# Kernel tuning notes

Measured on AMD Instinct MI355X. Metric: run time of the kernel, lower is better.

## Reference

```python
import jax, jax.numpy as jnp
import numpy as np

C, V, L, P, E, HM, H, M, B, T = 512, 32000, 2, 2, 8, 1024, 8, 256, 2, 1024
TOPK, RATIO = 2, 0.5


def setup_inputs() -> dict:
    key = jax.random.key(0)
    ks = iter(jax.random.split(key, 64))

    def nrm(shape, s=0.02):
        return (jax.random.normal(next(ks), shape) * s).astype(jnp.float32)

    return {
        "ids": jax.random.randint(next(ks), (B, T), 0, V, dtype=jnp.int32),
        "embed_w": nrm((V, C)),
        "mem": nrm((M, C)),
        "mp_w": nrm((2 * C, C)), "mp_b": jnp.zeros((C,), jnp.float32),
        "qkv_w": nrm((L, P, C, 3 * C)), "qkv_b": jnp.zeros((L, P, 3 * C), jnp.float32),
        "aw_w": nrm((L, P, C, H)), "aw_b": jnp.zeros((L, P, H), jnp.float32),
        "dscale": jnp.ones((L, P), jnp.float32),
        "mg_w": nrm((L, P * C, C)), "mg_b": jnp.zeros((L, C), jnp.float32),
        "ln_g": jnp.ones((L, C), jnp.float32), "ln_b": jnp.zeros((L, C), jnp.float32),
        "gw": nrm((L, C, E)), "gb": jnp.zeros((L, E), jnp.float32),
        "ew1": nrm((L, E, C, HM)), "eb1": jnp.zeros((L, E, HM), jnp.float32),
        "ew2": nrm((L, E, HM, C)), "eb2": jnp.zeros((L, E, C), jnp.float32),
        "q1w": nrm((L, C, 4 * C)), "q1b": jnp.zeros((L, 4 * C), jnp.float32),
        "q2w": nrm((L, 4 * C, 1)), "q2b": jnp.zeros((L, 1), jnp.float32),
        "errw": nrm((L, C, C)), "errb": jnp.zeros((L, C), jnp.float32),
        "ag1w": nrm((2 * C, 4 * C)), "ag1b": jnp.zeros((4 * C,), jnp.float32),
        "ag2w": nrm((4 * C, C)), "ag2b": jnp.zeros((C,), jnp.float32),
        "pscale": jnp.ones((C,), jnp.float32),
        "head_w": nrm((C, V)), "head_b": jnp.zeros((V,), jnp.float32),
    }


def _forward(ids, embed_w, mem, mp_w, mp_b, qkv_w, qkv_b, aw_w, aw_b, dscale,
             mg_w, mg_b, ln_g, ln_b, gw, gb, ew1, eb1, ew2, eb2,
             q1w, q1b, q2w, q2b, errw, errb, ag1w, ag1b, ag2w, ag2b,
             pscale, head_w, head_b):
    b, t = ids.shape
    hd = C // H
    x = embed_w[ids]                                        # [B,T,C] embedding gather
    # DynamicMemoryBank: attention over memory slots, concat retrieved
    en = jnp.einsum('btc,mc->btm', x, mem)
    ret = jnp.einsum('btm,mc->btc', jax.nn.softmax(en, -1), mem)
    x = jnp.concatenate([x, ret], -1) @ mp_w + mp_b         # memory_proj
    for l in range(L):
        x_in = x
        # IterativeReasoningBlock: stacked MetaCognitiveAttention phases
        h = x_in
        prior = None
        outs = []
        for p in range(P):
            qkv = (h @ qkv_w[l, p] + qkv_b[l, p]).reshape(b, t, 3, H, hd)
            q, k, v = (jnp.moveaxis(qkv[:, :, i], 1, 2) for i in range(3))  # [B,H,T,hd]
            aware = (h.mean(1) @ aw_w[l, p] + aw_b[l, p])[:, :, None, None]  # [B,H,1,1]
            attn = jax.nn.softmax(
                jnp.einsum('bhtd,bhsd->bhts', q, k) * (dscale[l, p] * aware), -1)
            if prior is not None:
                attn = attn + 0.3 * prior
            prior = jax.lax.stop_gradient(attn)
            o = jnp.einsum('bhts,bhsd->bthd', attn, v).reshape(b, t, C)
            h = jax.nn.silu(o)
            outs.append(h)
        merged = jnp.concatenate(outs, -1) @ mg_w[l] + mg_b[l]
        z = merged + x_in
        mu = z.mean(-1, keepdims=True)
        xn = (z - mu) / jnp.sqrt(z.var(-1, keepdims=True) + 1e-5) * ln_g[l] + ln_b[l]
        # MoE: softmax gate, top-k routing, combine (dense-equivalent math)
        scores = jax.nn.softmax(xn @ gw[l] + gb[l], -1)     # [B,T,E]
        vals, idx = jax.lax.top_k(scores, TOPK)
        w = jnp.sum(jax.nn.one_hot(idx, E, dtype=xn.dtype) * vals[..., None], axis=-2)
        eh = jnp.einsum('btc,ech->bteh', xn, ew1[l]) + eb1[l]
        eh = eh * jax.nn.silu(eh)                           # swiglu act: x*silu(x)
        ey = jnp.einsum('bteh,ehc->btec', eh, ew2[l]) + eb2[l]
        moe_out = jnp.einsum('btec,bte->btc', ey, w)
        reason = xn + moe_out * RATIO
        # IntrospectionLayer (quality estimator sees detached x)
        quality = jax.nn.sigmoid(
            jax.nn.silu(jax.lax.stop_gradient(x_in) @ q1w[l] + q1b[l]) @ q2w[l] + q2b[l])
        intro = x_in + 0.3 * ((x_in * (1.0 - quality)) @ errw[l] + errb[l])
        # AutonomousLearningGate
        gate = jnp.tanh(
            jax.nn.silu(jnp.concatenate([reason, intro], -1) @ ag1w + ag1b) @ ag2w + ag2b)
        x = reason + gate * pscale * intro
    return x @ head_w + head_b                              # [B,T,V]


def reference(ids, embed_w, mem, mp_w, mp_b, qkv_w, qkv_b, aw_w, aw_b, dscale,
              mg_w, mg_b, ln_g, ln_b, gw, gb, ew1, eb1, ew2, eb2,
              q1w, q1b, q2w, q2b, errw, errb, ag1w, ag1b, ag2w, ag2b,
              pscale, head_w, head_b):
    return _forward(ids, embed_w, mem, mp_w, mp_b, qkv_w, qkv_b, aw_w, aw_b, dscale,
                    mg_w, mg_b, ln_g, ln_b, gw, gb, ew1, eb1, ew2, eb2,
                    q1w, q1b, q2w, q2b, errw, errb, ag1w, ag1b, ag2w, ag2b,
                    pscale, head_w, head_b)
```

## Files before the change

### kernel.cpp

```cpp
#include <hip/hip_runtime.h>


#define NTOK 2048
#define CDIM 512
#define TLEN 1024
#define NB 2
#define NH 8
#define VDIM 32000

typedef __attribute__((ext_vector_type(4))) float f32x4;
typedef __attribute__((ext_vector_type(8))) __bf16 bf16x8;

#define AS1 __attribute__((address_space(1)))
#define AS3 __attribute__((address_space(3)))

__device__ __forceinline__ void g2lds16(const void* g, void* l) {
    __builtin_amdgcn_global_load_lds((const AS1 void*)g, (AS3 void*)l, 16, 0, 0);
}

__global__ __launch_bounds__(256) void gemm_bf16(
    const __bf16* __restrict__ A,
    const __bf16* __restrict__ B,
    float* __restrict__ C_, int ldc,
    const float* __restrict__ bias,
    const float* __restrict__ res, int ldres, float alpha,
    int K, int act)
{
    __shared__ __bf16 As[128 * 32];
    __shared__ __bf16 Bs[128 * 32];
    const int tid = threadIdx.x;
    const int w = tid >> 6, lane = tid & 63;
    const int m0 = blockIdx.y * 128, n0 = blockIdx.x * 128;
    const int wr = (w >> 1) * 64, wc = (w & 1) * 64;
    f32x4 acc[4][4] = {};
    const int mrow = lane & 15, kq = (lane >> 4) * 8;
    for (int k0 = 0; k0 < K; k0 += 32) {
#pragma unroll
        for (int i = 0; i < 2; ++i) {
            const int boff = w * 2048 + i * 1024 + lane * 16;
            const int row = boff >> 6;
            const int ke = (boff & 63) >> 1;
            g2lds16(A + (long)(m0 + row) * K + k0 + ke, (char*)As + (boff - lane * 16));
            g2lds16(B + (long)(n0 + row) * K + k0 + ke, (char*)Bs + (boff - lane * 16));
        }
        __syncthreads();
        bf16x8 af[4], bfr[4];
#pragma unroll
        for (int i = 0; i < 4; ++i)
            af[i] = *(const bf16x8*)(As + (wr + i * 16 + mrow) * 32 + kq);
#pragma unroll
        for (int j = 0; j < 4; ++j)
            bfr[j] = *(const bf16x8*)(Bs + (wc + j * 16 + mrow) * 32 + kq);
#pragma unroll
        for (int i = 0; i < 4; ++i)
#pragma unroll
            for (int j = 0; j < 4; ++j)
                acc[i][j] = __builtin_amdgcn_mfma_f32_16x16x32_bf16(af[i], bfr[j], acc[i][j], 0, 0, 0);
        __syncthreads();
    }
    const int col_l = lane & 15, row_l = (lane >> 4) * 4;
#pragma unroll
    for (int i = 0; i < 4; ++i)
#pragma unroll
        for (int j = 0; j < 4; ++j) {
            const int n = n0 + wc + j * 16 + col_l;
            const float bv = bias ? bias[n] : 0.f;
#pragma unroll
            for (int r = 0; r < 4; ++r) {
                const int m = m0 + wr + i * 16 + row_l + r;
                float v = acc[i][j][r] + bv;
                if (act == 1) v = v / (1.f + __expf(-v));
                else if (act == 2) v = tanhf(v);
                v *= alpha;
                if (res) v += res[(long)m * ldres + n];
                C_[(long)m * ldc + n] = v;
            }
        }
}

__global__ __launch_bounds__(256) void route_k(const int* __restrict__ eidx,
                                               int* __restrict__ offi,
                                               int* __restrict__ list,
                                               int* __restrict__ posmap)
{
    __shared__ int cnt[8], fill[8], seg[9];
    const int t = threadIdx.x;
    if (t < 8) cnt[t] = 0;
    __syncthreads();
    for (int i = t; i < NTOK * 2; i += 256) atomicAdd(&cnt[eidx[i]], 1);
    __syncthreads();
    if (t == 0) {
        int run = 0;
        for (int e = 0; e < 8; ++e) {
            seg[e] = run;
            run += (cnt[e] + 127) & ~127;
        }
        seg[8] = run;
    }
    __syncthreads();
    if (t < 8) fill[t] = seg[t];
    if (t < 9) offi[t] = seg[t];
    __syncthreads();
    for (int i = t; i < NTOK * 2; i += 256) {
        const int e = eidx[i];
        const int g = atomicAdd(&fill[e], 1);
        list[g] = i;
        posmap[i] = g;
    }
    __syncthreads();
#pragma unroll
    for (int e = 0; e < 8; ++e)
        for (int g = seg[e] + cnt[e] + t; g < seg[e + 1]; g += 256) list[g] = 0;
}

__global__ __launch_bounds__(256) void moe_g1_k(
    const __bf16* __restrict__ A,
    const __bf16* __restrict__ Bw,
    const float* __restrict__ eb1l,
    const int* __restrict__ offi,
    const int* __restrict__ list,
    __bf16* __restrict__ EHB)
{
    const int m0 = blockIdx.y * 128;
    if (m0 >= offi[8]) return;
    int e = 0;
    while (e < 7 && offi[e + 1] <= m0) ++e;
    const __bf16* B = Bw + (long)e * (1024 * 512);
    const float* bias = eb1l + e * 1024;
    __shared__ __bf16 As[128 * 32];
    __shared__ __bf16 Bs[128 * 32];
    __shared__ int toks[128];
    const int tid = threadIdx.x;
    if (tid < 128) toks[tid] = list[m0 + tid] >> 1;
    __syncthreads();
    const int w = tid >> 6, lane = tid & 63;
    const int n0 = blockIdx.x * 128;
    const int wr = (w >> 1) * 64, wc = (w & 1) * 64;
    f32x4 acc[4][4] = {};
    const int mrow = lane & 15, kq = (lane >> 4) * 8;
    for (int k0 = 0; k0 < 512; k0 += 32) {
#pragma unroll
        for (int i = 0; i < 2; ++i) {
            const int boff = w * 2048 + i * 1024 + lane * 16;
            const int row = boff >> 6;
            const int ke = (boff & 63) >> 1;
            g2lds16(A + (long)toks[row] * 512 + k0 + ke, (char*)As + (boff - lane * 16));
            g2lds16(B + (long)(n0 + row) * 512 + k0 + ke, (char*)Bs + (boff - lane * 16));
        }
        __syncthreads();
        bf16x8 af[4], bfr[4];
#pragma unroll
        for (int i = 0; i < 4; ++i)
            af[i] = *(const bf16x8*)(As + (wr + i * 16 + mrow) * 32 + kq);
#pragma unroll
        for (int j = 0; j < 4; ++j)
            bfr[j] = *(const bf16x8*)(Bs + (wc + j * 16 + mrow) * 32 + kq);
#pragma unroll
        for (int i = 0; i < 4; ++i)
#pragma unroll
            for (int j = 0; j < 4; ++j)
                acc[i][j] = __builtin_amdgcn_mfma_f32_16x16x32_bf16(af[i], bfr[j], acc[i][j], 0, 0, 0);
        __syncthreads();
    }
    const int col_l = lane & 15, row_l = (lane >> 4) * 4;
#pragma unroll
    for (int i = 0; i < 4; ++i)
#pragma unroll
        for (int j = 0; j < 4; ++j) {
            const int n = n0 + wc + j * 16 + col_l;
            const float bv = bias[n];
#pragma unroll
            for (int r = 0; r < 4; ++r) {
                const int g = m0 + wr + i * 16 + row_l + r;
                const float v = acc[i][j][r] + bv;
                EHB[(long)g * 1024 + n] = (__bf16)(v * v / (1.f + __expf(-v)));
            }
        }
}

__global__ __launch_bounds__(256) void moe_g2_k(
    const __bf16* __restrict__ A,
    const __bf16* __restrict__ Bw,
    const float* __restrict__ eb2l,
    const int* __restrict__ offi,
    float* __restrict__ EYS)
{
    const int m0 = blockIdx.y * 128;
    if (m0 >= offi[8]) return;
    int e = 0;
    while (e < 7 && offi[e + 1] <= m0) ++e;
    const __bf16* B = Bw + (long)e * (512 * 1024);
    const float* bias = eb2l + e * 512;
    __shared__ __bf16 As[128 * 32];
    __shared__ __bf16 Bs[128 * 32];
    const int tid = threadIdx.x;
    const int w = tid >> 6, lane = tid & 63;
    const int n0 = blockIdx.x * 128;
    const int wr = (w >> 1) * 64, wc = (w & 1) * 64;
    f32x4 acc[4][4] = {};
    const int mrow = lane & 15, kq = (lane >> 4) * 8;
    for (int k0 = 0; k0 < 1024; k0 += 32) {
#pragma unroll
        for (int i = 0; i < 2; ++i) {
            const int boff = w * 2048 + i * 1024 + lane * 16;
            const int row = boff >> 6;
            const int ke = (boff & 63) >> 1;
            g2lds16(A + (long)(m0 + row) * 1024 + k0 + ke, (char*)As + (boff - lane * 16));
            g2lds16(B + (long)(n0 + row) * 1024 + k0 + ke, (char*)Bs + (boff - lane * 16));
        }
        __syncthreads();
        bf16x8 af[4], bfr[4];
#pragma unroll
        for (int i = 0; i < 4; ++i)
            af[i] = *(const bf16x8*)(As + (wr + i * 16 + mrow) * 32 + kq);
#pragma unroll
        for (int j = 0; j < 4; ++j)
            bfr[j] = *(const bf16x8*)(Bs + (wc + j * 16 + mrow) * 32 + kq);
#pragma unroll
        for (int i = 0; i < 4; ++i)
#pragma unroll
            for (int j = 0; j < 4; ++j)
                acc[i][j] = __builtin_amdgcn_mfma_f32_16x16x32_bf16(af[i], bfr[j], acc[i][j], 0, 0, 0);
        __syncthreads();
    }
    const int col_l = lane & 15, row_l = (lane >> 4) * 4;
#pragma unroll
    for (int i = 0; i < 4; ++i)
#pragma unroll
        for (int j = 0; j < 4; ++j) {
            const int n = n0 + wc + j * 16 + col_l;
            const float bv = bias[n];
#pragma unroll
            for (int r = 0; r < 4; ++r) {
                const int g = m0 + wr + i * 16 + row_l + r;
                EYS[(long)g * 512 + n] = acc[i][j][r] + bv;
            }
        }
}

__global__ __launch_bounds__(256) void reason2_k(const float* __restrict__ xn,
                                                 const float* __restrict__ EYS,
                                                 const float* __restrict__ wv,
                                                 const int* __restrict__ posmap,
                                                 float* __restrict__ reason)
{
    const long i = (long)blockIdx.x * 256 + threadIdx.x;
    const long n = i >> 9;
    const int c = (int)(i & 511);
    const int g0 = posmap[n * 2], g1 = posmap[n * 2 + 1];
    const float v = wv[n * 2] * EYS[(long)g0 * 512 + c] + wv[n * 2 + 1] * EYS[(long)g1 * 512 + c];
    reason[i] = xn[i] + 0.5f * v;
}

__global__ __launch_bounds__(256) void wtrans_k(const float* __restrict__ W0,
                                                __bf16* __restrict__ Wt0, int K, int N,
                                                long sW, long sD)
{
    const float* W = W0 + (long)blockIdx.z * sW;
    __bf16* Wt = Wt0 + (long)blockIdx.z * sD;
    __shared__ float tile[64][65];
    const int k0 = blockIdx.y * 64, n0 = blockIdx.x * 64;
    const int t = threadIdx.x;
#pragma unroll
    for (int i = 0; i < 4; ++i) {
        const int r = (t >> 4) + i * 16;
        const int c = (t & 15) * 4;
        float4 v = *(const float4*)(W + (long)(k0 + r) * N + n0 + c);
        tile[r][c] = v.x; tile[r][c + 1] = v.y; tile[r][c + 2] = v.z; tile[r][c + 3] = v.w;
    }
    __syncthreads();
#pragma unroll
    for (int i = 0; i < 4; ++i) {
        const int rr = (t >> 4) + i * 16;
        const int cc = (t & 15) * 4;
        __bf16* o = Wt + (long)(n0 + rr) * K + k0 + cc;
        o[0] = (__bf16)tile[cc][rr];
        o[1] = (__bf16)tile[cc + 1][rr];
        o[2] = (__bf16)tile[cc + 2][rr];
        o[3] = (__bf16)tile[cc + 3][rr];
    }
}

__global__ __launch_bounds__(256) void cvta_k(const float* __restrict__ src, int lda, int K,
                                              __bf16* __restrict__ dst)
{
    const int row = blockIdx.x, t = threadIdx.x;
    const float* s = src + (long)row * lda;
    __bf16* d = dst + (long)row * K;
    for (int c = t * 4; c < K; c += 1024) {
        float4 v = *(const float4*)(s + c);
        d[c] = (__bf16)v.x; d[c + 1] = (__bf16)v.y; d[c + 2] = (__bf16)v.z; d[c + 3] = (__bf16)v.w;
    }
}

__global__ __launch_bounds__(256) void embed_k(const int* __restrict__ ids,
                                               const float* __restrict__ ew,
                                               float* __restrict__ x)
{
    const int n = blockIdx.x, t = threadIdx.x;
    const long r = (long)ids[n] * CDIM;
    x[(long)n * CDIM + t]       = ew[r + t];
    x[(long)n * CDIM + 256 + t] = ew[r + 256 + t];
}

__global__ __launch_bounds__(256) void smrows_k(float* __restrict__ a)
{
    const int n = blockIdx.x, t = threadIdx.x;
    __shared__ float rs[256];
    float v = a[(long)n * 256 + t];
    rs[t] = v; __syncthreads();
    for (int o = 128; o; o >>= 1) { if (t < o) rs[t] = fmaxf(rs[t], rs[t + o]); __syncthreads(); }
    const float m = rs[0]; __syncthreads();
    const float e = __expf(v - m);
    rs[t] = e; __syncthreads();
    for (int o = 128; o; o >>= 1) { if (t < o) rs[t] += rs[t + o]; __syncthreads(); }
    a[(long)n * 256 + t] = e / rs[0];
}

__global__ __launch_bounds__(256) void concat_k(const float* __restrict__ a,
                                                const float* __restrict__ b,
                                                float* __restrict__ o)
{
    const long i = (long)blockIdx.x * 256 + threadIdx.x;
    const long n = i >> 9;
    const int c = (int)(i & 511);
    o[n * 1024 + c]       = a[i];
    o[n * 1024 + 512 + c] = b[i];
}

__global__ __launch_bounds__(64) void meanp_k(const float* __restrict__ A, int lda,
                                              float* __restrict__ part)
{
    const int bid = blockIdx.x;
    const int ts = bid & 15;
    const int cg = (bid >> 4) & 7;
    const int b  = bid >> 7;
    const int c  = cg * 64 + threadIdx.x;
    const float* p = A + ((long)b * TLEN + ts * 64) * lda + c;
    float s = 0.f;
    for (int t = 0; t < 64; ++t) s += p[(long)t * lda];
    part[(long)ts * 1024 + b * 512 + c] = s;
}
__global__ __launch_bounds__(256) void meanr_k(const float* __restrict__ part,
                                               float* __restrict__ hm)
{
    const int i = blockIdx.x * 256 + threadIdx.x;
    float s = 0.f;
    for (int ts = 0; ts < 16; ++ts) s += part[ts * 1024 + i];
    hm[i] = s * (1.f / 1024.f);
}

__global__ __launch_bounds__(64) void aware_k(const float* __restrict__ hm,
                                              const float* __restrict__ aw_w,
                                              const float* __restrict__ aw_b,
                                              int lp, float* __restrict__ out)
{
    const int t = threadIdx.x;
    if (t < NB * NH) {
        const int b = t >> 3, hh = t & 7;
        const float* W = aw_w + (long)lp * CDIM * NH;
        const float* x = hm + b * CDIM;
        float s = aw_b[lp * NH + hh];
        for (int c = 0; c < CDIM; ++c) s += x[c] * W[c * NH + hh];
        out[t] = s;
    }
}

__global__ __launch_bounds__(256) void qkvprep_k(
    const float* __restrict__ qkv,
    const float* __restrict__ dscale, int lp,
    const float* __restrict__ aware,
    __bf16* __restrict__ QKB, __bf16* __restrict__ KB, __bf16* __restrict__ VTB)
{
    const int bh = blockIdx.x >> 4;
    const int tc = blockIdx.x & 15;
    const int b = bh >> 3, h = bh & 7;
    const int tid = threadIdx.x;
    const float sc = dscale[lp] * aware[bh];
    __shared__ float vt[64][68];
    const int row = tid >> 2, c0 = (tid & 3) * 16;
    const long rbase = ((long)(b * 1024 + tc * 64 + row)) * 1536 + h * 64 + c0;
    {
        bf16x8 qo[2], ko[2];
#pragma unroll
        for (int i = 0; i < 2; ++i)
#pragma unroll
            for (int jj = 0; jj < 2; ++jj) {
                const float4 qq = *(const float4*)(qkv + rbase + (i * 2 + jj) * 4);
                const float4 kk = *(const float4*)(qkv + rbase + 512 + (i * 2 + jj) * 4);
                qo[i][jj * 4 + 0] = (__bf16)(qq.x * sc);
                qo[i][jj * 4 + 1] = (__bf16)(qq.y * sc);
                qo[i][jj * 4 + 2] = (__bf16)(qq.z * sc);
                qo[i][jj * 4 + 3] = (__bf16)(qq.w * sc);
                ko[i][jj * 4 + 0] = (__bf16)kk.x;
                ko[i][jj * 4 + 1] = (__bf16)kk.y;
                ko[i][jj * 4 + 2] = (__bf16)kk.z;
                ko[i][jj * 4 + 3] = (__bf16)kk.w;
            }
        const long obase = (long)bh * 65536 + (long)(tc * 64 + row) * 64 + c0;
        *(bf16x8*)(QKB + obase) = qo[0];
        *(bf16x8*)(QKB + obase + 8) = qo[1];
        *(bf16x8*)(KB + obase) = ko[0];
        *(bf16x8*)(KB + obase + 8) = ko[1];
    }
    {
        const long vbase = ((long)(b * 1024 + tc * 64 + row)) * 1536 + 1024 + h * 64 + c0;
#pragma unroll
        for (int i = 0; i < 4; ++i) {
            const float4 v = *(const float4*)(qkv + vbase + i * 4);
            vt[row][c0 + i * 4 + 0] = v.x;
            vt[row][c0 + i * 4 + 1] = v.y;
            vt[row][c0 + i * 4 + 2] = v.z;
            vt[row][c0 + i * 4 + 3] = v.w;
        }
    }
    __syncthreads();
    {
        const int d = row;
        const int s0 = c0;
        bf16x8 o0, o1;
#pragma unroll
        for (int j = 0; j < 8; ++j) o0[j] = (__bf16)vt[s0 + j][d];
#pragma unroll
        for (int j = 0; j < 8; ++j) o1[j] = (__bf16)vt[s0 + 8 + j][d];
        __bf16* dst = VTB + (long)bh * 65536 + (long)d * 1024 + tc * 64 + s0;
        *(bf16x8*)dst = o0;
        *(bf16x8*)(dst + 8) = o1;
    }
}

#define RB 32
__global__ __launch_bounds__(256) void attn2_k(
    const __bf16* __restrict__ QKB,
    const __bf16* __restrict__ KB,
    const __bf16* __restrict__ VTB,
    __bf16* __restrict__ prior,
    int use_prior,
    float* __restrict__ outs, int out_off)
{
    __shared__ __align__(16) __bf16 qs[RB * 64];
    __shared__ __align__(16) __bf16 kv[2][128 * 64];
    __shared__ __align__(16) __bf16 ss[RB * 1024];
    const int tid = threadIdx.x;
    const int w = tid >> 6, lane = tid & 63;
    const int rb = blockIdx.x & 31;
    const int bh = blockIdx.x >> 5;
    const int b = bh >> 3, h = bh & 7;
    const int t0 = rb * RB;
    const long qkbase = (long)bh * 65536;
    const int mrow = lane & 15, kq = (lane >> 4) * 8;

    {
        const int row = tid >> 3, gl = tid & 7;
        const int gs = gl ^ (row & 7);
        g2lds16(QKB + qkbase + (long)(t0 + row) * 64 + gs * 8,
                (char*)qs + tid * 16 - lane * 16);
    }
    {
        for (int it = 0; it < 4; ++it) {
            const int idx = it * 256 + tid;
            const int row = idx >> 3, gl = idx & 7;
            const int gs = gl ^ (row & 7);
            g2lds16(KB + qkbase + (long)row * 64 + gs * 8,
                    (char*)kv[0] + idx * 16 - lane * 16);
        }
        __syncthreads();
        int buf = 0;
        const int ntb = w * 2;
        for (int c = 0; c < 8; ++c) {
            if (c < 7) {
                const int s0n = (c + 1) * 128;
                for (int it = 0; it < 4; ++it) {
                    const int idx = it * 256 + tid;
                    const int row = idx >> 3, gl = idx & 7;
                    const int gs = gl ^ (row & 7);
                    g2lds16(KB + qkbase + (long)(s0n + row) * 64 + gs * 8,
                            (char*)kv[buf ^ 1] + idx * 16 - lane * 16);
                }
            }
            f32x4 accs[2][2] = {};
#pragma unroll
            for (int k0 = 0; k0 < 64; k0 += 32) {
                bf16x8 aq[2], bk[2];
#pragma unroll
                for (int mt = 0; mt < 2; ++mt) {
                    const int r = mt * 16 + mrow;
                    const int col = k0 + kq;
                    aq[mt] = *(const bf16x8*)(qs + r * 64 + (((col >> 3) ^ (r & 7)) << 3));
                }
#pragma unroll
                for (int j = 0; j < 2; ++j) {
                    const int nl = (ntb + j) * 16 + mrow;
                    const int col = k0 + kq;
                    bk[j] = *(const bf16x8*)(kv[buf] + nl * 64 + (((col >> 3) ^ (nl & 7)) << 3));
                }
#pragma unroll
                for (int mt = 0; mt < 2; ++mt)
#pragma unroll
                    for (int j = 0; j < 2; ++j)
                        accs[mt][j] = __builtin_amdgcn_mfma_f32_16x16x32_bf16(aq[mt], bk[j], accs[mt][j], 0, 0, 0);
            }
            const int col_l = lane & 15, row_l = (lane >> 4) * 4;
#pragma unroll
            for (int mt = 0; mt < 2; ++mt)
#pragma unroll
                for (int j = 0; j < 2; ++j) {
                    const int ccol = c * 128 + (ntb + j) * 16 + col_l;
#pragma unroll
                    for (int r = 0; r < 4; ++r) {
                        const int rr = mt * 16 + row_l + r;
                        ss[rr * 1024 + (((ccol >> 3) ^ (rr & 7)) << 3) + (ccol & 7)] = (__bf16)accs[mt][j][r];
                    }
                }
            __syncthreads();
            buf ^= 1;
        }
    }
    for (int it = 0; it < 4; ++it) {
        const int idx = it * 256 + tid;
        const int d = idx >> 4, gl = idx & 15;
        const int gs = gl ^ (d & 7);
        g2lds16(VTB + (long)bh * 65536 + (long)d * 1024 + gs * 8,
                (char*)kv[0] + idx * 16 - lane * 16);
    }
    {
        const int r = tid >> 3;
        const int li = tid & 7;
        const int rsw = r & 7;
        float mx = -1e30f;
        for (int j = 0; j < 16; ++j) {
            const int c = j * 64 + li * 8;
            bf16x8 v = *(const bf16x8*)(ss + r * 1024 + (((c >> 3) ^ rsw) << 3));
#pragma unroll
            for (int q = 0; q < 8; ++q) mx = fmaxf(mx, (float)v[q]);
        }
        mx = fmaxf(mx, __shfl_xor(mx, 1));
        mx = fmaxf(mx, __shfl_xor(mx, 2));
        mx = fmaxf(mx, __shfl_xor(mx, 4));
        float sum = 0.f;
        for (int j = 0; j < 16; ++j) {
            const int c = j * 64 + li * 8;
            __bf16* p = ss + r * 1024 + (((c >> 3) ^ rsw) << 3);
            bf16x8 v = *(const bf16x8*)p;
            bf16x8 e;
#pragma unroll
            for (int q = 0; q < 8; ++q) {
                const float ev = __expf((float)v[q] - mx);
                sum += ev;
                e[q] = (__bf16)ev;
            }
            *(bf16x8*)p = e;
        }
        sum += __shfl_xor(sum, 1);
        sum += __shfl_xor(sum, 2);
        sum += __shfl_xor(sum, 4);
        const float rinv = 1.f / sum;
        const long pbase = ((long)bh * 1024 + t0 + r) * 1024;
        for (int j = 0; j < 16; ++j) {
            const int c = j * 64 + li * 8;
            __bf16* p = ss + r * 1024 + (((c >> 3) ^ rsw) << 3);
            bf16x8 v = *(const bf16x8*)p;
            bf16x8 o;
            if (use_prior) {
                bf16x8 pr = *(const bf16x8*)(prior + pbase + c);
#pragma unroll
                for (int q = 0; q < 8; ++q)
                    o[q] = (__bf16)((float)v[q] * rinv + 0.3f * (float)pr[q]);
            } else {
#pragma unroll
                for (int q = 0; q < 8; ++q)
                    o[q] = (__bf16)((float)v[q] * rinv);
            }
            *(bf16x8*)p = o;
            *(bf16x8*)(prior + pbase + c) = o;
        }
    }
    __syncthreads();
    {
        f32x4 po[2] = {};
        int buf = 0;
        const int mt = w >> 1;
        const int ntb2 = (w & 1) * 2;
        for (int c = 0; c < 8; ++c) {
            if (c < 7) {
                const int s0n = (c + 1) * 128;
                for (int it = 0; it < 4; ++it) {
                    const int idx = it * 256 + tid;
                    const int d = idx >> 4, gl = idx & 15;
                    const int gs = gl ^ (d & 7);
                    g2lds16(VTB + (long)bh * 65536 + (long)d * 1024 + s0n + gs * 8,
                            (char*)kv[buf ^ 1] + idx * 16 - lane * 16);
                }
            }
#pragma unroll
            for (int ks = 0; ks < 4; ++ks) {
                const int r = mt * 16 + mrow;
                const int cola = c * 128 + ks * 32 + kq;
                bf16x8 pa = *(const bf16x8*)(ss + r * 1024 + (((cola >> 3) ^ (r & 7)) << 3));
                bf16x8 vb[2];
#pragma unroll
                for (int j = 0; j < 2; ++j) {
                    const int d = (ntb2 + j) * 16 + mrow;
                    const int colv = ks * 32 + kq;
                    vb[j] = *(const bf16x8*)(kv[buf] + d * 128 + (((colv >> 3) ^ (d & 7)) << 3));
                }
                po[0] = __builtin_amdgcn_mfma_f32_16x16x32_bf16(pa, vb[0], po[0], 0, 0, 0);
                po[1] = __builtin_amdgcn_mfma_f32_16x16x32_bf16(pa, vb[1], po[1], 0, 0, 0);
            }
            __syncthreads();
            buf ^= 1;
        }
        const int col_l = lane & 15, row_l = (lane >> 4) * 4;
#pragma unroll
        for (int j = 0; j < 2; ++j) {
            const int d = out_off + h * 64 + (ntb2 + j) * 16 + col_l;
#pragma unroll
            for (int r = 0; r < 4; ++r) {
                const int trow = t0 + mt * 16 + row_l + r;
                float v = po[j][r];
                v = v / (1.f + __expf(-v));
                outs[((long)(b * 1024 + trow)) * 1024 + d] = v;
            }
        }
    }
}

__global__ __launch_bounds__(256) void ln_k(const float* __restrict__ z,
                                            const float* __restrict__ g,
                                            const float* __restrict__ bb,
                                            float* __restrict__ xn)
{
    const int n = blockIdx.x, t = threadIdx.x;
    __shared__ float rs[256], rq[256];
    const float v0 = z[(long)n * 512 + t];
    const float v1 = z[(long)n * 512 + 256 + t];
    rs[t] = v0 + v1;
    rq[t] = v0 * v0 + v1 * v1;
    __syncthreads();
    for (int o = 128; o; o >>= 1) {
        if (t < o) { rs[t] += rs[t + o]; rq[t] += rq[t + o]; }
        __syncthreads();
    }
    const float mu = rs[0] * (1.f / 512.f);
    const float var = rq[0] * (1.f / 512.f) - mu * mu;
    const float rstd = rsqrtf(var + 1e-5f);
    xn[(long)n * 512 + t]       = (v0 - mu) * rstd * g[t] + bb[t];
    xn[(long)n * 512 + 256 + t] = (v1 - mu) * rstd * g[t + 256] + bb[t + 256];
}

__global__ __launch_bounds__(64) void gate_k(const float* __restrict__ xn,
                                             const float* __restrict__ gw,
                                             const float* __restrict__ gb,
                                             int l, float* __restrict__ wv,
                                             int* __restrict__ eidx)
{
    const int n = blockIdx.x, t = threadIdx.x;
    const int e = t & 7, ch = t >> 3;
    const float* W = gw + (long)l * CDIM * 8;
    float part = 0.f;
    for (int k = ch * 64; k < ch * 64 + 64; ++k) part += xn[(long)n * CDIM + k] * W[k * 8 + e];
    part += __shfl_xor(part, 8, 64);
    part += __shfl_xor(part, 16, 64);
    part += __shfl_xor(part, 32, 64);
    __shared__ float lg[8];
    if (t < 8) lg[t] = part + gb[l * 8 + t];
    __syncthreads();
    if (t == 0) {
        float m = lg[0];
        for (int i = 1; i < 8; ++i) m = fmaxf(m, lg[i]);
        float p[8], s = 0.f;
        for (int i = 0; i < 8; ++i) { p[i] = __expf(lg[i] - m); s += p[i]; }
        const float inv = 1.f / s;
        int i0 = 0;
        for (int i = 1; i < 8; ++i) if (p[i] > p[i0]) i0 = i;
        int i1 = (i0 == 0) ? 1 : 0;
        for (int i = 0; i < 8; ++i) { if (i == i0) continue; if (p[i] > p[i1]) i1 = i; }
        eidx[n * 2] = i0; eidx[n * 2 + 1] = i1;
        wv[n * 2] = p[i0] * inv; wv[n * 2 + 1] = p[i1] * inv;
    }
}

__global__ __launch_bounds__(256) void qual_k(const float* __restrict__ t1,
                                              const float* __restrict__ q2w,
                                              const float* __restrict__ q2b,
                                              int l, float* __restrict__ qual)
{
    const int n = blockIdx.x, t = threadIdx.x;
    const float* W = q2w + (long)l * 2048;
    float s = 0.f;
    for (int k = t; k < 2048; k += 256) s += t1[(long)n * 2048 + k] * W[k];
    __shared__ float rs[256];
    rs[t] = s; __syncthreads();
    for (int o = 128; o; o >>= 1) { if (t < o) rs[t] += rs[t + o]; __syncthreads(); }
    if (t == 0) {
        const float q = rs[0] + q2b[l];
        qual[n] = 1.f / (1.f + __expf(-q));
    }
}

__global__ __launch_bounds__(256) void xq_k(const float* __restrict__ x_in,
                                            const float* __restrict__ qual,
                                            float* __restrict__ xq)
{
    const long i = (long)blockIdx.x * 256 + threadIdx.x;
    const long n = i >> 9;
    xq[i] = x_in[i] * (1.f - qual[n]);
}

__global__ __launch_bounds__(256) void final_k(const float* __restrict__ reason,
                                               const float* __restrict__ gate,
                                               const float* __restrict__ pscale,
                                               const float* __restrict__ intro,
                                               float* __restrict__ xo)
{
    const long i = (long)blockIdx.x * 256 + threadIdx.x;
    const int c = (int)(i & 511);
    xo[i] = reason[i] + gate[i] * pscale[c] * intro[i];
}

extern "C" void kernel_launch(void* const* d_in, const int* in_sizes, int n_in,
                              void* d_out, int out_size, void* d_ws, size_t ws_size,
                              hipStream_t stream)
{
    (void)in_sizes; (void)n_in; (void)out_size; (void)ws_size;
    const int*   ids     = (const int*)  d_in[0];
    const float* embed_w = (const float*)d_in[1];
    const float* mem     = (const float*)d_in[2];
    const float* mp_w    = (const float*)d_in[3];
    const float* mp_b    = (const float*)d_in[4];
    const float* qkv_w   = (const float*)d_in[5];
    const float* qkv_b   = (const float*)d_in[6];
    const float* aw_w    = (const float*)d_in[7];
    const float* aw_b    = (const float*)d_in[8];
    const float* dscale  = (const float*)d_in[9];
    const float* mg_w    = (const float*)d_in[10];
    const float* mg_b    = (const float*)d_in[11];
    const float* ln_g    = (const float*)d_in[12];
    const float* ln_b    = (const float*)d_in[13];
    const float* gw      = (const float*)d_in[14];
    const float* gb      = (const float*)d_in[15];
    const float* ew1     = (const float*)d_in[16];
    const float* eb1     = (const float*)d_in[17];
    const float* ew2     = (const float*)d_in[18];
    const float* eb2     = (const float*)d_in[19];
    const float* q1w     = (const float*)d_in[20];
    const float* q1b     = (const float*)d_in[21];
    const float* q2w     = (const float*)d_in[22];
    const float* q2b     = (const float*)d_in[23];
    const float* errw    = (const float*)d_in[24];
    const float* errb    = (const float*)d_in[25];
    const float* ag1w    = (const float*)d_in[26];
    const float* ag1b    = (const float*)d_in[27];
    const float* ag2w    = (const float*)d_in[28];
    const float* ag2b    = (const float*)d_in[29];
    const float* pscale  = (const float*)d_in[30];
    const float* head_w  = (const float*)d_in[31];
    const float* head_b  = (const float*)d_in[32];
    float* out = (float*)d_out;
    float* ws  = (float*)d_ws;

    const long NC = (long)NTOK * CDIM;
    float* X0   = ws;
    float* X1   = ws + NC;
    float* RET  = ws + 2 * NC;
    float* XCAT = ws + 3 * NC;
    float* QKV  = ws + 5 * NC;
    float* OUTS = ws + 8 * NC;
    float* EN   = ws + 10 * NC;
    float* SM   = ws + 10 * NC + NC / 2;
    float* PART = SM;
    float* HMEAN= SM + 16384;
    float* AWARE= SM + 17408;
    float* QUAL = SM + 17472;
    float* WV   = SM + 19520;
    int*   EIDX = (int*)(SM + 23616);
    int*   OFFI = (int*)(SM + 27712);
    int*   LIST = (int*)(SM + 27728);
    int*   POSMAP = (int*)(SM + 32848);
    float* R      = ws + 11 * NC;
    __bf16* PRIORB = (__bf16*)R;
    float* Z      = R;
    float* XN     = R + NC;
    float* REASON = R + 2 * NC;
    float* INTRO  = R + 3 * NC;
    float* XQ     = R + 4 * NC;
    float* GATEB  = R + 5 * NC;
    __bf16* EHB   = (__bf16*)(R + 6 * NC);
    float* EYS    = R + 9 * NC;
    float* Q1B    = R + 12 * NC;

    __bf16* bfw = (__bf16*)(ws + 27 * NC);
    __bf16* WB_mp   = bfw;
    __bf16* WB_qkv  = bfw + 524288;
    __bf16* WB_mg   = bfw + 3670016;
    __bf16* WB_q1   = bfw + 4718592;
    __bf16* WB_err  = bfw + 6815744;
    __bf16* WB_ag1  = bfw + 7340032;
    __bf16* WB_ag2  = bfw + 9437184;
    __bf16* WB_memn = bfw + 10485760;
    __bf16* WB_memt = bfw + 10616832;
    __bf16* WB_head = bfw + 10747904;
    __bf16* ABF     = bfw + 27131904;
    __bf16* WB_e1   = bfw + 31326208;
    __bf16* WB_e2   = bfw + 39714816;
    __bf16* QKB = ABF;
    __bf16* KB  = ABF + 1048576;
    __bf16* VTB = ABF + 2097152;

    auto wtransN = [&](const float* W, __bf16* Wt, int K, int N, int cnt, long sW, long sD) {
        wtrans_k<<<dim3(N / 64, K / 64, cnt), 256, 0, stream>>>(W, Wt, K, N, sW, sD);
    };
    auto gemm = [&](const float* Asrc, int lda, const __bf16* B, float* C_, int ldc,
                    const float* bias, const float* res, int ldres, float alpha,
                    int Nn, int K, int act) {
        cvta_k<<<NTOK, 256, 0, stream>>>(Asrc, lda, K, ABF);
        gemm_bf16<<<dim3(Nn / 128, NTOK / 128), 256, 0, stream>>>(
            ABF, B, C_, ldc, bias, res, ldres, alpha, K, act);
    };

    wtransN(mp_w, WB_mp, 1024, 512, 1, 0, 0);
    wtransN(qkv_w, WB_qkv, 512, 1536, 4, 512 * 1536, 1536 * 512);
    wtransN(mg_w, WB_mg, 1024, 512, 2, 1024 * 512, 512 * 1024);
    wtransN(q1w, WB_q1, 512, 2048, 2, 512 * 2048, 2048 * 512);
    wtransN(errw, WB_err, 512, 512, 2, 512 * 512, 512 * 512);
    wtransN(ew1, WB_e1, 512, 1024, 16, 524288, 524288);
    wtransN(ew2, WB_e2, 1024, 512, 16, 524288, 524288);
    wtransN(ag1w, WB_ag1, 1024, 2048, 1, 0, 0);
    wtransN(ag2w, WB_ag2, 2048, 512, 1, 0, 0);
    wtransN(head_w, WB_head, 512, VDIM, 1, 0, 0);
    wtransN(mem, WB_memt, 256, 512, 1, 0, 0);
    cvta_k<<<256, 256, 0, stream>>>(mem, 512, 512, WB_memn);

    embed_k<<<NTOK, 256, 0, stream>>>(ids, embed_w, X0);
    gemm(X0, 512, WB_memn, EN, 256, nullptr, nullptr, 0, 1.f, 256, 512, 0);
    smrows_k<<<NTOK, 256, 0, stream>>>(EN);
    gemm(EN, 256, WB_memt, RET, 512, nullptr, nullptr, 0, 1.f, 512, 256, 0);
    concat_k<<<4096, 256, 0, stream>>>(X0, RET, XCAT);
    gemm(XCAT, 1024, WB_mp, X0, 512, mp_b, nullptr, 0, 1.f, 512, 1024, 0);

    float* xcur = X0;
    float* xalt = X1;
    for (int l = 0; l < 2; ++l) {
        for (int p = 0; p < 2; ++p) {
            const int lp = l * 2 + p;
            const float* hptr = (p == 0) ? xcur : OUTS;
            const int hlda = (p == 0) ? 512 : 1024;
            gemm(hptr, hlda, WB_qkv + (long)lp * 1536 * 512, QKV, 1536,
                 qkv_b + (long)lp * 1536, nullptr, 0, 1.f, 1536, 512, 0);
            meanp_k<<<256, 64, 0, stream>>>(hptr, hlda, PART);
            meanr_k<<<4, 256, 0, stream>>>(PART, HMEAN);
            aware_k<<<1, 64, 0, stream>>>(HMEAN, aw_w, aw_b, lp, AWARE);
            qkvprep_k<<<256, 256, 0, stream>>>(QKV, dscale, lp, AWARE, QKB, KB, VTB);
            attn2_k<<<512, 256, 0, stream>>>(QKB, KB, VTB, PRIORB,
                                             (p == 1) ? 1 : 0, OUTS, p * CDIM);
        }
        gemm(OUTS, 1024, WB_mg + (long)l * 512 * 1024, Z, 512, mg_b + (long)l * 512,
             xcur, 512, 1.f, 512, 1024, 0);
        ln_k<<<NTOK, 256, 0, stream>>>(Z, ln_g + (long)l * 512, ln_b + (long)l * 512, XN);
        gate_k<<<NTOK, 64, 0, stream>>>(XN, gw, gb, l, WV, EIDX);
        route_k<<<1, 256, 0, stream>>>(EIDX, OFFI, LIST, POSMAP);
        cvta_k<<<NTOK, 256, 0, stream>>>(XN, 512, 512, ABF);
        moe_g1_k<<<dim3(8, 40), 256, 0, stream>>>(ABF, WB_e1 + (long)l * 8 * 524288,
                eb1 + (long)l * 8192, OFFI, LIST, EHB);
        moe_g2_k<<<dim3(4, 40), 256, 0, stream>>>(EHB, WB_e2 + (long)l * 8 * 524288,
                eb2 + (long)l * 4096, OFFI, EYS);
        reason2_k<<<4096, 256, 0, stream>>>(XN, EYS, WV, POSMAP, REASON);
        gemm(xcur, 512, WB_q1 + (long)l * 2048 * 512, Q1B, 2048, q1b + (long)l * 2048,
             nullptr, 0, 1.f, 2048, 512, 1);
        qual_k<<<NTOK, 256, 0, stream>>>(Q1B, q2w, q2b, l, QUAL);
        xq_k<<<4096, 256, 0, stream>>>(xcur, QUAL, XQ);
        gemm(XQ, 512, WB_err + (long)l * 512 * 512, INTRO, 512, errb + (long)l * 512,
             xcur, 512, 0.3f, 512, 512, 0);
        concat_k<<<4096, 256, 0, stream>>>(REASON, INTRO, XCAT);
        gemm(XCAT, 1024, WB_ag1, Q1B, 2048, ag1b, nullptr, 0, 1.f, 2048, 1024, 1);
        gemm(Q1B, 2048, WB_ag2, GATEB, 512, ag2b, nullptr, 0, 1.f, 512, 2048, 2);
        final_k<<<4096, 256, 0, stream>>>(REASON, GATEB, pscale, INTRO, xalt);
        float* tmp = xcur; xcur = xalt; xalt = tmp;
    }
    gemm(xcur, 512, WB_head, out, VDIM, head_b, nullptr, 0, 1.f, VDIM, 512, 0);
}
```

Before: 1.695 ms.

## Fuse bf16 conversions into producer epilogues and add XCD-aware GEMM tile swizzle

Every GEMM used to start with a separate cvta_k pass converting its fp32 activation to bf16. Producers (embed, softmax, attention, layernorm, xq, final, GEMM epilogues) now write bf16 copies directly, so those conversion launches and their extra round trips through memory go away. Intermediates that are only consumed as GEMM inputs, such as the Q1 and ag1 outputs, are stored only in bf16. The GEMM grid becomes 1D with blocks remapped so consecutive tiles land on the same XCD for better L2 reuse. Some producers now do extra bf16 stores, and qual_k reads a bf16 input, which slightly lowers its precision.

```diff
diff --git a/kernel.cpp b/kernel.cpp
--- a/kernel.cpp
+++ b/kernel.cpp
@@ -19,9 +19,10 @@
 }
 
 __global__ __launch_bounds__(256) void gemm_bf16(
-    const __bf16* __restrict__ A,
+    const __bf16* __restrict__ A, int lda,
     const __bf16* __restrict__ B,
     float* __restrict__ C_, int ldc,
+    __bf16* __restrict__ Cb, int ldcb,
     const float* __restrict__ bias,
     const float* __restrict__ res, int ldres, float alpha,
     int K, int act)
@@ -30,7 +31,11 @@
     __shared__ __bf16 Bs[128 * 32];
     const int tid = threadIdx.x;
     const int w = tid >> 6, lane = tid & 63;
-    const int m0 = blockIdx.y * 128, n0 = blockIdx.x * 128;
+    const int nwg = gridDim.x;
+    const int q = nwg >> 3, r = nwg & 7;
+    const int xcd = blockIdx.x & 7, ii = blockIdx.x >> 3;
+    const int swz = (xcd < r) ? xcd * (q + 1) + ii : r * (q + 1) + (xcd - r) * q + ii;
+    const int m0 = (swz & 15) * 128, n0 = (swz >> 4) * 128;
     const int wr = (w >> 1) * 64, wc = (w & 1) * 64;
     f32x4 acc[4][4] = {};
     const int mrow = lane & 15, kq = (lane >> 4) * 8;
@@ -40,7 +45,7 @@
             const int boff = w * 2048 + i * 1024 + lane * 16;
             const int row = boff >> 6;
             const int ke = (boff & 63) >> 1;
-            g2lds16(A + (long)(m0 + row) * K + k0 + ke, (char*)As + (boff - lane * 16));
+            g2lds16(A + (long)(m0 + row) * lda + k0 + ke, (char*)As + (boff - lane * 16));
             g2lds16(B + (long)(n0 + row) * K + k0 + ke, (char*)Bs + (boff - lane * 16));
         }
         __syncthreads();
@@ -66,14 +71,15 @@
             const int n = n0 + wc + j * 16 + col_l;
             const float bv = bias ? bias[n] : 0.f;
 #pragma unroll
-            for (int r = 0; r < 4; ++r) {
-                const int m = m0 + wr + i * 16 + row_l + r;
-                float v = acc[i][j][r] + bv;
+            for (int r2 = 0; r2 < 4; ++r2) {
+                const int m = m0 + wr + i * 16 + row_l + r2;
+                float v = acc[i][j][r2] + bv;
                 if (act == 1) v = v / (1.f + __expf(-v));
                 else if (act == 2) v = tanhf(v);
                 v *= alpha;
                 if (res) v += res[(long)m * ldres + n];
-                C_[(long)m * ldc + n] = v;
+                if (C_) C_[(long)m * ldc + n] = v;
+                if (Cb) Cb[(long)m * ldcb + n] = (__bf16)v;
             }
         }
 }
@@ -295,15 +301,20 @@
 
 __global__ __launch_bounds__(256) void embed_k(const int* __restrict__ ids,
                                                const float* __restrict__ ew,
-                                               float* __restrict__ x)
+                                               float* __restrict__ x,
+                                               __bf16* __restrict__ xb)
 {
     const int n = blockIdx.x, t = threadIdx.x;
     const long r = (long)ids[n] * CDIM;
-    x[(long)n * CDIM + t]       = ew[r + t];
-    x[(long)n * CDIM + 256 + t] = ew[r + 256 + t];
-}
-
-__global__ __launch_bounds__(256) void smrows_k(float* __restrict__ a)
+    const float v0 = ew[r + t], v1 = ew[r + 256 + t];
+    x[(long)n * CDIM + t]       = v0;
+    x[(long)n * CDIM + 256 + t] = v1;
+    xb[(long)n * CDIM + t]       = (__bf16)v0;
+    xb[(long)n * CDIM + 256 + t] = (__bf16)v1;
+}
+
+__global__ __launch_bounds__(256) void smrows_k(const float* __restrict__ a,
+                                                __bf16* __restrict__ ob)
 {
     const int n = blockIdx.x, t = threadIdx.x;
     __shared__ float rs[256];
@@ -314,18 +325,18 @@
     const float e = __expf(v - m);
     rs[t] = e; __syncthreads();
     for (int o = 128; o; o >>= 1) { if (t < o) rs[t] += rs[t + o]; __syncthreads(); }
-    a[(long)n * 256 + t] = e / rs[0];
-}
-
-__global__ __launch_bounds__(256) void concat_k(const float* __restrict__ a,
-                                                const float* __restrict__ b,
-                                                float* __restrict__ o)
+    ob[(long)n * 256 + t] = (__bf16)(e / rs[0]);
+}
+
+__global__ __launch_bounds__(256) void concat_bf_k(const float* __restrict__ a,
+                                                   const float* __restrict__ b,
+                                                   __bf16* __restrict__ o)
 {
     const long i = (long)blockIdx.x * 256 + threadIdx.x;
     const long n = i >> 9;
     const int c = (int)(i & 511);
-    o[n * 1024 + c]       = a[i];
-    o[n * 1024 + 512 + c] = b[i];
+    o[n * 1024 + c]       = (__bf16)a[i];
+    o[n * 1024 + 512 + c] = (__bf16)b[i];
 }
 
 __global__ __launch_bounds__(64) void meanp_k(const float* __restrict__ A, int lda,
@@ -436,7 +447,7 @@
     const __bf16* __restrict__ VTB,
     __bf16* __restrict__ prior,
     int use_prior,
-    float* __restrict__ outs, int out_off)
+    float* __restrict__ outs, __bf16* __restrict__ outsb, int out_off)
 {
     __shared__ __align__(16) __bf16 qs[RB * 64];
     __shared__ __align__(16) __bf16 kv[2][128 * 64];
@@ -619,7 +630,9 @@
                 const int trow = t0 + mt * 16 + row_l + r;
                 float v = po[j][r];
                 v = v / (1.f + __expf(-v));
-                outs[((long)(b * 1024 + trow)) * 1024 + d] = v;
+                const long oi = ((long)(b * 1024 + trow)) * 1024 + d;
+                outs[oi] = v;
+                outsb[oi] = (__bf16)v;
             }
         }
     }
@@ -628,7 +641,8 @@
 __global__ __launch_bounds__(256) void ln_k(const float* __restrict__ z,
                                             const float* __restrict__ g,
                                             const float* __restrict__ bb,
-                                            float* __restrict__ xn)
+                                            float* __restrict__ xn,
+                                            __bf16* __restrict__ xnb)
 {
     const int n = blockIdx.x, t = threadIdx.x;
     __shared__ float rs[256], rq[256];
@@ -644,8 +658,12 @@
     const float mu = rs[0] * (1.f / 512.f);
     const float var = rq[0] * (1.f / 512.f) - mu * mu;
     const float rstd = rsqrtf(var + 1e-5f);
-    xn[(long)n * 512 + t]       = (v0 - mu) * rstd * g[t] + bb[t];
-    xn[(long)n * 512 + 256 + t] = (v1 - mu) * rstd * g[t + 256] + bb[t + 256];
+    const float o0 = (v0 - mu) * rstd * g[t] + bb[t];
+    const float o1 = (v1 - mu) * rstd * g[t + 256] + bb[t + 256];
+    xn[(long)n * 512 + t]       = o0;
+    xn[(long)n * 512 + 256 + t] = o1;
+    xnb[(long)n * 512 + t]       = (__bf16)o0;
+    xnb[(long)n * 512 + 256 + t] = (__bf16)o1;
 }
 
 __global__ __launch_bounds__(64) void gate_k(const float* __restrict__ xn,
@@ -680,7 +698,7 @@
     }
 }
 
-__global__ __launch_bounds__(256) void qual_k(const float* __restrict__ t1,
+__global__ __launch_bounds__(256) void qual_k(const __bf16* __restrict__ t1,
                                               const float* __restrict__ q2w,
                                               const float* __restrict__ q2b,
                                               int l, float* __restrict__ qual)
@@ -688,7 +706,7 @@
     const int n = blockIdx.x, t = threadIdx.x;
     const float* W = q2w + (long)l * 2048;
     float s = 0.f;
-    for (int k = t; k < 2048; k += 256) s += t1[(long)n * 2048 + k] * W[k];
+    for (int k = t; k < 2048; k += 256) s += (float)t1[(long)n * 2048 + k] * W[k];
     __shared__ float rs[256];
     rs[t] = s; __syncthreads();
     for (int o = 128; o; o >>= 1) { if (t < o) rs[t] += rs[t + o]; __syncthreads(); }
@@ -700,22 +718,25 @@
 
 __global__ __launch_bounds__(256) void xq_k(const float* __restrict__ x_in,
                                             const float* __restrict__ qual,
-                                            float* __restrict__ xq)
+                                            __bf16* __restrict__ xqb)
 {
     const long i = (long)blockIdx.x * 256 + threadIdx.x;
     const long n = i >> 9;
-    xq[i] = x_in[i] * (1.f - qual[n]);
+    xqb[i] = (__bf16)(x_in[i] * (1.f - qual[n]));
 }
 
 __global__ __launch_bounds__(256) void final_k(const float* __restrict__ reason,
                                                const float* __restrict__ gate,
                                                const float* __restrict__ pscale,
                                                const float* __restrict__ intro,
-                                               float* __restrict__ xo)
+                                               float* __restrict__ xo,
+                                               __bf16* __restrict__ xob)
 {
     const long i = (long)blockIdx.x * 256 + threadIdx.x;
     const int c = (int)(i & 511);
-    xo[i] = reason[i] + gate[i] * pscale[c] * intro[i];
+    const float v = reason[i] + gate[i] * pscale[c] * intro[i];
+    xo[i] = v;
+    xob[i] = (__bf16)v;
 }
 
 extern "C" void kernel_launch(void* const* d_in, const int* in_sizes, int n_in,
@@ -763,7 +784,6 @@
     float* X0   = ws;
     float* X1   = ws + NC;
     float* RET  = ws + 2 * NC;
-    float* XCAT = ws + 3 * NC;
     float* QKV  = ws + 5 * NC;
     float* OUTS = ws + 8 * NC;
     float* EN   = ws + 10 * NC;
@@ -783,11 +803,9 @@
     float* XN     = R + NC;
     float* REASON = R + 2 * NC;
     float* INTRO  = R + 3 * NC;
-    float* XQ     = R + 4 * NC;
     float* GATEB  = R + 5 * NC;
     __bf16* EHB   = (__bf16*)(R + 6 * NC);
     float* EYS    = R + 9 * NC;
-    float* Q1B    = R + 12 * NC;
 
     __bf16* bfw = (__bf16*)(ws + 27 * NC);
     __bf16* WB_mp   = bfw;
@@ -800,22 +818,28 @@
     __bf16* WB_memn = bfw + 10485760;
     __bf16* WB_memt = bfw + 10616832;
     __bf16* WB_head = bfw + 10747904;
-    __bf16* ABF     = bfw + 27131904;
+    __bf16* QKB = bfw + 27131904;
+    __bf16* KB  = QKB + 1048576;
+    __bf16* VTB = KB + 1048576;
     __bf16* WB_e1   = bfw + 31326208;
     __bf16* WB_e2   = bfw + 39714816;
-    __bf16* QKB = ABF;
-    __bf16* KB  = ABF + 1048576;
-    __bf16* VTB = ABF + 2097152;
+    __bf16* X0B   = bfw + 48103424;
+    __bf16* X1B   = X0B + 1048576;
+    __bf16* XCATB = X1B + 1048576;
+    __bf16* OUTSB = XCATB + 2097152;
+    __bf16* XNB   = OUTSB + 2097152;
+    __bf16* XQB   = XNB + 1048576;
+    __bf16* Q1BB  = XQB + 1048576;
+    __bf16* ENB   = Q1BB + 4194304;
 
     auto wtransN = [&](const float* W, __bf16* Wt, int K, int N, int cnt, long sW, long sD) {
         wtrans_k<<<dim3(N / 64, K / 64, cnt), 256, 0, stream>>>(W, Wt, K, N, sW, sD);
     };
-    auto gemm = [&](const float* Asrc, int lda, const __bf16* B, float* C_, int ldc,
-                    const float* bias, const float* res, int ldres, float alpha,
-                    int Nn, int K, int act) {
-        cvta_k<<<NTOK, 256, 0, stream>>>(Asrc, lda, K, ABF);
-        gemm_bf16<<<dim3(Nn / 128, NTOK / 128), 256, 0, stream>>>(
-            ABF, B, C_, ldc, bias, res, ldres, alpha, K, act);
+    auto gemm = [&](const __bf16* A, int lda, const __bf16* Bm, float* C_, int ldc,
+                    __bf16* Cb, int ldcb, const float* bias, const float* res, int ldres,
+                    float alpha, int Nn, int K, int act) {
+        gemm_bf16<<<(Nn / 128) * 16, 256, 0, stream>>>(
+            A, lda, Bm, C_, ldc, Cb, ldcb, bias, res, ldres, alpha, K, act);
     };
 
     wtransN(mp_w, WB_mp, 1024, 512, 1, 0, 0);
@@ -831,51 +855,54 @@
     wtransN(mem, WB_memt, 256, 512, 1, 0, 0);
     cvta_k<<<256, 256, 0, stream>>>(mem, 512, 512, WB_memn);
 
-    embed_k<<<NTOK, 256, 0, stream>>>(ids, embed_w, X0);
-    gemm(X0, 512, WB_memn, EN, 256, nullptr, nullptr, 0, 1.f, 256, 512, 0);
-    smrows_k<<<NTOK, 256, 0, stream>>>(EN);
-    gemm(EN, 256, WB_memt, RET, 512, nullptr, nullptr, 0, 1.f, 512, 256, 0);
-    concat_k<<<4096, 256, 0, stream>>>(X0, RET, XCAT);
-    gemm(XCAT, 1024, WB_mp, X0, 512, mp_b, nullptr, 0, 1.f, 512, 1024, 0);
+    embed_k<<<NTOK, 256, 0, stream>>>(ids, embed_w, X0, X0B);
+    gemm(X0B, 512, WB_memn, EN, 256, nullptr, 0, nullptr, nullptr, 0, 1.f, 256, 512, 0);
+    smrows_k<<<NTOK, 256, 0, stream>>>(EN, ENB);
+    gemm(ENB, 256, WB_memt, RET, 512, nullptr, 0, nullptr, nullptr, 0, 1.f, 512, 256, 0);
+    concat_bf_k<<<4096, 256, 0, stream>>>(X0, RET, XCATB);
+    gemm(XCATB, 1024, WB_mp, X0, 512, X0B, 512, mp_b, nullptr, 0, 1.f, 512, 1024, 0);
 
     float* xcur = X0;
     float* xalt = X1;
+    __bf16* xcurB = X0B;
+    __bf16* xaltB = X1B;
     for (int l = 0; l < 2; ++l) {
         for (int p = 0; p < 2; ++p) {
             const int lp = l * 2 + p;
             const float* hptr = (p == 0) ? xcur : OUTS;
+            const __bf16* hptrB = (p == 0) ? xcurB : OUTSB;
             const int hlda = (p == 0) ? 512 : 1024;
-            gemm(hptr, hlda, WB_qkv + (long)lp * 1536 * 512, QKV, 1536,
+            gemm(hptrB, hlda, WB_qkv + (long)lp * 1536 * 512, QKV, 1536, nullptr, 0,
                  qkv_b + (long)lp * 1536, nullptr, 0, 1.f, 1536, 512, 0);
             meanp_k<<<256, 64, 0, stream>>>(hptr, hlda, PART);
             meanr_k<<<4, 256, 0, stream>>>(PART, HMEAN);
             aware_k<<<1, 64, 0, stream>>>(HMEAN, aw_w, aw_b, lp, AWARE);
             qkvprep_k<<<256, 256, 0, stream>>>(QKV, dscale, lp, AWARE, QKB, KB, VTB);
             attn2_k<<<512, 256, 0, stream>>>(QKB, KB, VTB, PRIORB,
-                                             (p == 1) ? 1 : 0, OUTS, p * CDIM);
-        }
-        gemm(OUTS, 1024, WB_mg + (long)l * 512 * 1024, Z, 512, mg_b + (long)l * 512,
-             xcur, 512, 1.f, 512, 1024, 0);
-        ln_k<<<NTOK, 256, 0, stream>>>(Z, ln_g + (long)l * 512, ln_b + (long)l * 512, XN);
+                                             (p == 1) ? 1 : 0, OUTS, OUTSB, p * CDIM);
+        }
+        gemm(OUTSB, 1024, WB_mg + (long)l * 512 * 1024, Z, 512, nullptr, 0,
+             mg_b + (long)l * 512, xcur, 512, 1.f, 512, 1024, 0);
+        ln_k<<<NTOK, 256, 0, stream>>>(Z, ln_g + (long)l * 512, ln_b + (long)l * 512, XN, XNB);
         gate_k<<<NTOK, 64, 0, stream>>>(XN, gw, gb, l, WV, EIDX);
         route_k<<<1, 256, 0, stream>>>(EIDX, OFFI, LIST, POSMAP);
-        cvta_k<<<NTOK, 256, 0, stream>>>(XN, 512, 512, ABF);
-        moe_g1_k<<<dim3(8, 40), 256, 0, stream>>>(ABF, WB_e1 + (long)l * 8 * 524288,
+        moe_g1_k<<<dim3(8, 40), 256, 0, stream>>>(XNB, WB_e1 + (long)l * 8 * 524288,
                 eb1 + (long)l * 8192, OFFI, LIST, EHB);
         moe_g2_k<<<dim3(4, 40), 256, 0, stream>>>(EHB, WB_e2 + (long)l * 8 * 524288,
                 eb2 + (long)l * 4096, OFFI, EYS);
         reason2_k<<<4096, 256, 0, stream>>>(XN, EYS, WV, POSMAP, REASON);
-        gemm(xcur, 512, WB_q1 + (long)l * 2048 * 512, Q1B, 2048, q1b + (long)l * 2048,
-             nullptr, 0, 1.f, 2048, 512, 1);
-        qual_k<<<NTOK, 256, 0, stream>>>(Q1B, q2w, q2b, l, QUAL);
-        xq_k<<<4096, 256, 0, stream>>>(xcur, QUAL, XQ);
-        gemm(XQ, 512, WB_err + (long)l * 512 * 512, INTRO, 512, errb + (long)l * 512,
-             xcur, 512, 0.3f, 512, 512, 0);
-        concat_k<<<4096, 256, 0, stream>>>(REASON, INTRO, XCAT);
-        gemm(XCAT, 1024, WB_ag1, Q1B, 2048, ag1b, nullptr, 0, 1.f, 2048, 1024, 1);
-        gemm(Q1B, 2048, WB_ag2, GATEB, 512, ag2b, nullptr, 0, 1.f, 512, 2048, 2);
-        final_k<<<4096, 256, 0, stream>>>(REASON, GATEB, pscale, INTRO, xalt);
+        gemm(xcurB, 512, WB_q1 + (long)l * 2048 * 512, nullptr, 0, Q1BB, 2048,
+             q1b + (long)l * 2048, nullptr, 0, 1.f, 2048, 512, 1);
+        qual_k<<<NTOK, 256, 0, stream>>>(Q1BB, q2w, q2b, l, QUAL);
+        xq_k<<<4096, 256, 0, stream>>>(xcur, QUAL, XQB);
+        gemm(XQB, 512, WB_err + (long)l * 512 * 512, INTRO, 512, nullptr, 0,
+             errb + (long)l * 512, xcur, 512, 0.3f, 512, 512, 0);
+        concat_bf_k<<<4096, 256, 0, stream>>>(REASON, INTRO, XCATB);
+        gemm(XCATB, 1024, WB_ag1, nullptr, 0, Q1BB, 2048, ag1b, nullptr, 0, 1.f, 2048, 1024, 1);
+        gemm(Q1BB, 2048, WB_ag2, GATEB, 512, nullptr, 0, ag2b, nullptr, 0, 1.f, 512, 2048, 2);
+        final_k<<<4096, 256, 0, stream>>>(REASON, GATEB, pscale, INTRO, xalt, xaltB);
         float* tmp = xcur; xcur = xalt; xalt = tmp;
-    }
-    gemm(xcur, 512, WB_head, out, VDIM, head_b, nullptr, 0, 1.f, VDIM, 512, 0);
-}
+        __bf16* tmpb = xcurB; xcurB = xaltB; xaltB = tmpb;
+    }
+    gemm(xcurB, 512, WB_head, out, VDIM, nullptr, 0, head_b, nullptr, 0, 1.f, VDIM, 512, 0);
+}
```

Result: no change. 1.679 ms (-0.9%).
